# Kernel optimization log

Measured on AMD Instinct MI355X. Metric: run time of the kernel, lower is better.

Reference implementation:

```python
import jax, jax.numpy as jnp
import numpy as np

B, S, D, E = 4, 2048, 1024, 8
HD = D // E          # per-expert head dim = 128
ROPE = HD // 2       # rotary dims = 64 (32 complex pairs)


def setup_inputs() -> dict:
    key = jax.random.key(0)
    ks = jax.random.split(key, 5)
    x = jax.random.normal(ks[0], (B, S, D), dtype=jnp.float32)
    Wg = jax.random.normal(ks[1], (D, E), dtype=jnp.float32) * 0.02
    Wqkv = jax.random.normal(ks[2], (E, D, 3 * HD), dtype=jnp.float32) * 0.02
    Wff = jax.random.normal(ks[3], (E, HD, D), dtype=jnp.float32) * 0.02
    b_ff = jnp.zeros((D,), dtype=jnp.float32)
    # precompute_freqs_cis(qk_rope_head_dim=ROPE, seqlen=S), theta=10000
    inv = 1.0 / (10000.0 ** (np.arange(0, ROPE, 2, dtype=np.float32) / ROPE))  # [ROPE//2]
    ang = np.arange(S, dtype=np.float32)[:, None] * inv[None, :]               # [S, ROPE//2]
    cos = jnp.asarray(np.cos(ang), dtype=jnp.float32)
    sin = jnp.asarray(np.sin(ang), dtype=jnp.float32)
    return {"x": x, "Wg": Wg, "Wqkv": Wqkv, "Wff": Wff, "b_ff": b_ff, "cos": cos, "sin": sin}


def _apply_rope(x, cos, sin):
    # x: [B,S,E,HD]; rotate the second half (x_pe), keep first half (x_nope), cat (pe, nope)
    b, s, e, hd = x.shape
    x_nope, x_pe = x[..., : hd // 2], x[..., hd // 2 :]
    xr = x_pe.reshape(b, s, e, hd // 4, 2)
    re, im = xr[..., 0], xr[..., 1]
    c = cos[None, :, None, :]
    sn = sin[None, :, None, :]
    rot = jnp.stack([re * c - im * sn, re * sn + im * c], axis=-1).reshape(b, s, e, hd // 2)
    return jnp.concatenate([rot, x_nope], axis=-1)


def reference(x, Wg, Wqkv, Wff, b_ff, cos, sin):
    b, s, d = x.shape
    e, hd = Wqkv.shape[0], Wqkv.shape[2] // 3
    # RoPE on per-expert chunks
    xh = _apply_rope(x.reshape(b, s, e, hd), cos, sin).reshape(b, s, d)
    # SwitchGate: top-1 routing
    probs = jax.nn.softmax(xh @ Wg, axis=-1)            # [b,s,E]
    expert = jnp.argmax(probs, axis=-1)                 # [b,s]
    gate = jnp.max(probs, axis=-1)                      # [b,s]
    # preprocess: per-expert stable gather of routed tokens (capacity = s, padded+masked)
    is_e = expert[None, :, :] == jnp.arange(e)[:, None, None]        # [E,b,s] bool
    order = jnp.argsort(jnp.where(is_e, 0, 1), axis=-1, stable=True)  # [E,b,s] routed-first
    mask_g = jnp.take_along_axis(is_e, order, axis=-1).astype(xh.dtype)  # [E,b,s]
    x_g = jnp.take_along_axis(xh[None], order[..., None], axis=2)    # [E,b,s,d]
    gate_g = jnp.take_along_axis(gate[None], order, axis=2)          # [E,b,s]
    # expert-grouped column-parallel QKV
    qkv = jnp.einsum("ebsd,edf->ebsf", x_g, Wqkv)                    # [E,b,s,3*hd]
    q, k, v = jnp.split(qkv, 3, axis=-1)                             # [E,b,s,hd]
    # grouped sparse attention within each expert's token set
    dot = jnp.einsum("ebqh,ebkh->ebqk", q, k) / jnp.sqrt(jnp.asarray(hd, xh.dtype))
    dot = dot - 1e6 * (1.0 - mask_g[:, :, None, :])
    attn = jax.nn.softmax(dot, axis=-1)
    ctx = jnp.einsum("ebqk,ebkh->ebqh", attn, v)                     # [E,b,s,hd]
    # row-parallel output projection, gate-weighted
    out = jnp.einsum("ebsh,ehd->ebsd", ctx, Wff) + b_ff
    out = out * (gate_g * mask_g)[..., None]
    # scatter_add combine back to [b,s,d]
    outs = jnp.zeros((b, s, d), dtype=xh.dtype)
    outs = outs.at[jnp.arange(b)[None, :, None], order].add(out)
    return outs
```

## Files before the change

### kernel.cpp

```cpp
#include <hip/hip_runtime.h>
#include <math.h>

#define Bn 4
#define Sn 2048
#define Dn 1024
#define En 8
#define HDn 128
#define NG 32
#define MAXT 160
#define MAXN 1024

typedef __attribute__((ext_vector_type(8))) short bf16x8;
typedef __attribute__((ext_vector_type(4))) float f32x4;
typedef unsigned short u16;

__device__ __forceinline__ unsigned bf16_rn(float x) {
  unsigned u = __float_as_uint(x);
  return (u + 0x7fffu + ((u >> 16) & 1u)) >> 16;
}
__device__ __forceinline__ void bsplit(float x, unsigned& hi, unsigned& lo) {
  hi = bf16_rn(x);
  lo = bf16_rn(x - __uint_as_float(hi << 16));
}
__device__ __forceinline__ void gl16(const void* g, void* l) {
  __builtin_amdgcn_global_load_lds(
      (const __attribute__((address_space(1))) void*)g,
      (__attribute__((address_space(3))) void*)l, 16, 0, 0);
}
#define MFMA16(a, b, c) __builtin_amdgcn_mfma_f32_16x16x32_bf16((a), (b), (c), 0, 0, 0)

__device__ __forceinline__ void prep_body(
    const float* __restrict__ W, u16* __restrict__ hiT, u16* __restrict__ loT,
    int Kdim, int Ndim, int e, int k0, int c0, float (*tile)[65])
{
  int t = threadIdx.x;
  int r = t >> 4, cc = (t & 15) << 2;
  const float* src = W + ((size_t)e * Kdim + k0) * Ndim + c0;
#pragma unroll
  for (int i = 0; i < 4; ++i) {
    float4 v = *(const float4*)(src + (size_t)(r + i * 16) * Ndim + cc);
    tile[r + i * 16][cc + 0] = v.x; tile[r + i * 16][cc + 1] = v.y;
    tile[r + i * 16][cc + 2] = v.z; tile[r + i * 16][cc + 3] = v.w;
  }
  __syncthreads();
#pragma unroll
  for (int i = 0; i < 4; ++i) {
    int oc = (t >> 4) + i * 16;
    int ok = (t & 15) << 2;
    float v0 = tile[ok + 0][oc], v1 = tile[ok + 1][oc];
    float v2 = tile[ok + 2][oc], v3 = tile[ok + 3][oc];
    unsigned h0,l0,h1,l1,h2,l2,h3,l3;
    bsplit(v0,h0,l0); bsplit(v1,h1,l1); bsplit(v2,h2,l2); bsplit(v3,h3,l3);
    size_t o = ((size_t)e * Ndim + c0 + oc) * Kdim + k0 + ok;
    *(ushort4*)(hiT + o) = make_ushort4((u16)h0,(u16)h1,(u16)h2,(u16)h3);
    *(ushort4*)(loT + o) = make_ushort4((u16)l0,(u16)l1,(u16)l2,(u16)l3);
  }
}

__global__ __launch_bounds__(256) void k_prologue(
    const float* __restrict__ x, const float* __restrict__ Wg,
    const float* __restrict__ cosT, const float* __restrict__ sinT,
    const float* __restrict__ Wqkv, const float* __restrict__ Wff,
    u16* __restrict__ xh_hi, u16* __restrict__ xh_lo,
    u16* __restrict__ WqT_hi, u16* __restrict__ WqT_lo,
    u16* __restrict__ WfT_hi, u16* __restrict__ WfT_lo,
    int* __restrict__ expertArr, float* __restrict__ gateArr,
    int* __restrict__ done)
{
  __shared__ float tile[64][65];
  int bid = blockIdx.x;
  if (bid == 0 && threadIdx.x == 0) done[0] = 0;
  if (bid < 2048) {
    int wid = threadIdx.x >> 6, l = threadIdx.x & 63;
    int bs = (bid << 2) + wid;
    int s  = bs & (Sn - 1);
    const float* xrow = x + (size_t)bs * Dn;
    int j0 = l << 4;
    int hb = j0 & ~127;
    int jj = j0 & 127;
    float v[16];
    if (jj < 64) {
      const float* pe = xrow + hb + 64 + jj;
      float a[16];
      *(float4*)(a + 0)  = *(const float4*)(pe + 0);
      *(float4*)(a + 4)  = *(const float4*)(pe + 4);
      *(float4*)(a + 8)  = *(const float4*)(pe + 8);
      *(float4*)(a + 12) = *(const float4*)(pe + 12);
      int p0 = jj >> 1;
#pragma unroll
      for (int i = 0; i < 8; ++i) {
        float c  = cosT[s * 32 + p0 + i];
        float sn = sinT[s * 32 + p0 + i];
        v[2 * i]     = a[2 * i] * c - a[2 * i + 1] * sn;
        v[2 * i + 1] = a[2 * i] * sn + a[2 * i + 1] * c;
      }
    } else {
      const float* np = xrow + hb + (jj - 64);
      *(float4*)(v + 0)  = *(const float4*)(np + 0);
      *(float4*)(v + 4)  = *(const float4*)(np + 4);
      *(float4*)(v + 8)  = *(const float4*)(np + 8);
      *(float4*)(v + 12) = *(const float4*)(np + 12);
    }
    u16 hh[16] __attribute__((aligned(16)));
    u16 ll[16] __attribute__((aligned(16)));
#pragma unroll
    for (int i = 0; i < 16; ++i) {
      unsigned h, lo;
      bsplit(v[i], h, lo);
      hh[i] = (u16)h; ll[i] = (u16)lo;
    }
    *(uint4*)(xh_hi + (size_t)bs * Dn + j0)     = *(uint4*)(hh);
    *(uint4*)(xh_hi + (size_t)bs * Dn + j0 + 8) = *(uint4*)(hh + 8);
    *(uint4*)(xh_lo + (size_t)bs * Dn + j0)     = *(uint4*)(ll);
    *(uint4*)(xh_lo + (size_t)bs * Dn + j0 + 8) = *(uint4*)(ll + 8);

    float pl[8] = {0.f, 0.f, 0.f, 0.f, 0.f, 0.f, 0.f, 0.f};
    const float* wr = Wg + (size_t)j0 * En;
#pragma unroll
    for (int i = 0; i < 16; ++i) {
      float4 w0 = *(const float4*)(wr + i * 8);
      float4 w1 = *(const float4*)(wr + i * 8 + 4);
      float xv = v[i];
      pl[0] += xv * w0.x; pl[1] += xv * w0.y; pl[2] += xv * w0.z; pl[3] += xv * w0.w;
      pl[4] += xv * w1.x; pl[5] += xv * w1.y; pl[6] += xv * w1.z; pl[7] += xv * w1.w;
    }
#pragma unroll
    for (int off = 1; off < 64; off <<= 1) {
#pragma unroll
      for (int e = 0; e < 8; ++e) pl[e] += __shfl_xor(pl[e], off, 64);
    }
    float m = pl[0]; int be = 0;
#pragma unroll
    for (int e = 1; e < 8; ++e) if (pl[e] > m) { m = pl[e]; be = e; }
    float ss = 0.f;
#pragma unroll
    for (int e = 0; e < 8; ++e) ss += expf(pl[e] - m);
    if (l == 0) {
      expertArr[bs] = be;
      gateArr[bs] = 1.0f / ss;
    }
  } else if (bid < 2048 + 768) {
    int id = bid - 2048;
    int e = id / 96, r2 = id % 96;
    prep_body(Wqkv, WqT_hi, WqT_lo, Dn, 384, e, (r2 / 6) << 6, (r2 % 6) << 6, tile);
  } else {
    int id = bid - 2816;
    int e = id >> 5, r2 = id & 31;
    prep_body(Wff, WfT_hi, WfT_lo, HDn, Dn, e, (r2 >> 4) << 6, (r2 & 15) << 6, tile);
  }
}

__global__ __launch_bounds__(256) void k_route(
    const int* __restrict__ expertArr, int* __restrict__ idx, int* __restrict__ cnt,
    int* __restrict__ tileg, int* __restrict__ tilem, int* __restrict__ ntile,
    int* __restrict__ done)
{
  int g = blockIdx.x;
  int b = g >> 3, e = g & 7;
  int t = threadIdx.x;
  __shared__ int wtot[4];
  __shared__ int base;
  if (t == 0) base = 0;
  __syncthreads();
  for (int c = 0; c < Sn; c += 256) {
    int s = c + t;
    int pred = (expertArr[b * Sn + s] == e) ? 1 : 0;
    unsigned long long mask = __ballot(pred);
    int ln = t & 63, wv = t >> 6;
    int wpre = __popcll(mask & ((1ull << ln) - 1ull));
    if (ln == 63) wtot[wv] = wpre + pred;
    __syncthreads();
    int woff = 0;
    for (int w = 0; w < wv; ++w) woff += wtot[w];
    int tot = wtot[0] + wtot[1] + wtot[2] + wtot[3];
    if (pred) idx[(g << 11) + base + woff + wpre] = s;
    __syncthreads();
    if (t == 0) base += tot;
    __syncthreads();
  }
  if (t == 0) {
    cnt[g] = base;
    __threadfence();
    if (atomicAdd(done, 1) == NG - 1) {
      int tc = 0;
      for (int gg = 0; gg < NG; ++gg) {
        int nn = __hip_atomic_load(&cnt[gg], __ATOMIC_ACQUIRE, __HIP_MEMORY_SCOPE_AGENT);
        for (int m0 = 0; m0 < nn && tc < MAXT; m0 += 64) { tileg[tc] = gg; tilem[tc] = m0; ++tc; }
      }
      ntile[0] = tc;
    }
  }
}

__global__ __launch_bounds__(256) void k_qkv(
    const u16* __restrict__ xh_hi, const u16* __restrict__ xh_lo,
    const u16* __restrict__ WqT_hi, const u16* __restrict__ WqT_lo,
    const int* __restrict__ idx, const int* __restrict__ cnt,
    u16* __restrict__ qkv_hi, u16* __restrict__ qkv_lo,
    u16* __restrict__ vT_hi, u16* __restrict__ vT_lo)
{
  extern __shared__ unsigned char LDS[];
  int bid = blockIdx.x;
  int r8 = bid & 7, q = bid >> 3;
  int g = r8 + ((q & 3) << 3);
  int slot = q >> 2;
  int m0 = (slot >> 1) << 6;
  int n0 = (slot & 1) * 192;
  int n = cnt[g];
  if (m0 >= n) return;
  int b = g >> 3, e = g & 7;
  const int* idxg = idx + (g << 11);
  int t = threadIdx.x;
  int w = t >> 6, l = t & 63;
  int lc = l & 15, lq = l >> 4;

  int srow = t >> 2;
  int sslot = (t & 3) ^ ((srow >> 1) & 3);
  int rgs = m0 + srow; rgs = rgs < n ? rgs : n - 1;
  size_t aoffR = ((size_t)(b * Sn + idxg[rgs])) * Dn + sslot * 8;
  size_t boffR0 = ((size_t)e * 384 + n0 + srow) * Dn + sslot * 8;
  unsigned dst = (unsigned)t << 4;

  f32x4 acc[4][3];
#pragma unroll
  for (int i = 0; i < 4; ++i)
#pragma unroll
    for (int j = 0; j < 3; ++j) acc[i][j] = (f32x4){0.f, 0.f, 0.f, 0.f};

  unsigned off = (unsigned)((lq ^ ((lc >> 1) & 3)) << 4);

#define STAGE(bb, k0)                                                 \
  do {                                                                \
    gl16(xh_hi + aoffR + (k0), LDS + (bb) + dst);                     \
    gl16(xh_lo + aoffR + (k0), LDS + (bb) + 4096 + dst);              \
    gl16(WqT_hi + boffR0 + (k0), LDS + (bb) + 8192 + dst);            \
    gl16(WqT_hi + boffR0 + (size_t)64 * Dn + (k0), LDS + (bb) + 12288 + dst); \
    gl16(WqT_hi + boffR0 + (size_t)128 * Dn + (k0), LDS + (bb) + 16384 + dst);\
    gl16(WqT_lo + boffR0 + (k0), LDS + (bb) + 20480 + dst);           \
    gl16(WqT_lo + boffR0 + (size_t)64 * Dn + (k0), LDS + (bb) + 24576 + dst); \
    gl16(WqT_lo + boffR0 + (size_t)128 * Dn + (k0), LDS + (bb) + 28672 + dst);\
  } while (0)

  STAGE(0, 0);
  asm volatile("s_waitcnt vmcnt(0)" ::: "memory");
  __builtin_amdgcn_s_barrier();
  for (int tt = 0; tt < 32; ++tt) {
    unsigned cur = (tt & 1) ? 32768u : 0u;
    if (tt < 31) {
      STAGE(cur ^ 32768u, (tt + 1) * 32);
      asm volatile("s_waitcnt vmcnt(8)" ::: "memory");
    } else {
      asm volatile("s_waitcnt vmcnt(0)" ::: "memory");
    }
    __builtin_amdgcn_s_barrier();
    bf16x8 ah[4], al[4], bh[3], bl[3];
#pragma unroll
    for (int fi = 0; fi < 4; ++fi) {
      unsigned ab = cur + (unsigned)((fi * 16 + lc) * 64) + off;
      ah[fi] = *(const bf16x8*)(LDS + ab);
      al[fi] = *(const bf16x8*)(LDS + ab + 4096);
    }
#pragma unroll
    for (int fj = 0; fj < 3; ++fj) {
      unsigned bb2 = cur + 8192u + (unsigned)((w * 48 + fj * 16 + lc) * 64) + off;
      bh[fj] = *(const bf16x8*)(LDS + bb2);
      bl[fj] = *(const bf16x8*)(LDS + bb2 + 12288);
    }
#pragma unroll
    for (int fi = 0; fi < 4; ++fi)
#pragma unroll
      for (int fj = 0; fj < 3; ++fj) {
        acc[fi][fj] = MFMA16(ah[fi], bh[fj], acc[fi][fj]);
        acc[fi][fj] = MFMA16(al[fi], bh[fj], acc[fi][fj]);
        acc[fi][fj] = MFMA16(ah[fi], bl[fj], acc[fi][fj]);
      }
    asm volatile("s_waitcnt lgkmcnt(0)" ::: "memory");
    __builtin_amdgcn_sched_barrier(0);
    __builtin_amdgcn_s_barrier();
  }
#undef STAGE

#pragma unroll
  for (int fi = 0; fi < 4; ++fi) {
#pragma unroll
    for (int rr = 0; rr < 4; ++rr) {
      int rg = m0 + fi * 16 + lq * 4 + rr;
      if (rg < n) {
        int tok = idxg[rg];
#pragma unroll
        for (int fj = 0; fj < 3; ++fj) {
          int col = n0 + w * 48 + fj * 16 + lc;
          unsigned h, lo2;
          bsplit(acc[fi][fj][rr], h, lo2);
          if (col < 256) {
            size_t o = (size_t)(b * Sn + tok) * 384 + col;
            qkv_hi[o] = (u16)h; qkv_lo[o] = (u16)lo2;
          } else {
            size_t o = ((size_t)g * HDn + (col - 256)) * MAXN + rg;
            vT_hi[o] = (u16)h; vT_lo[o] = (u16)lo2;
          }
        }
      }
    }
  }
}

__global__ __launch_bounds__(256) void k_attn(
    const u16* __restrict__ qkv_hi, const u16* __restrict__ qkv_lo,
    const u16* __restrict__ vT_hi, const u16* __restrict__ vT_lo,
    const int* __restrict__ idx, const int* __restrict__ cnt,
    const int* __restrict__ tileg, const int* __restrict__ tilem,
    const int* __restrict__ ntile,
    u16* __restrict__ ctx_hi, u16* __restrict__ ctx_lo)
{
  extern __shared__ unsigned char LDS[];
  int tid = blockIdx.x;
  if (tid >= ntile[0]) return;
  int g = tileg[tid], m0 = tilem[tid];
  int n = cnt[g];
  int b = g >> 3;
  const int* idxg = idx + (g << 11);
  int t = threadIdx.x, wid = t >> 6, l = t & 63;
  int lc = l & 15, lq = l >> 4;
  const float scale = 0.08838834764831845f;

  int qrg = m0 + wid * 16 + lc; qrg = qrg < n ? qrg : n - 1;
  size_t qoff = (size_t)(b * Sn + idxg[qrg]) * 384 + lq * 8;
  bf16x8 Qhi[4], Qlo[4];
#pragma unroll
  for (int ks = 0; ks < 4; ++ks) {
    Qhi[ks] = *(const bf16x8*)(qkv_hi + qoff + ks * 32);
    Qlo[ks] = *(const bf16x8*)(qkv_lo + qoff + ks * 32);
  }

  f32x4 acc[8];
#pragma unroll
  for (int i = 0; i < 8; ++i) acc[i] = (f32x4){0.f, 0.f, 0.f, 0.f};
  float m_r[4] = {-1e30f, -1e30f, -1e30f, -1e30f};
  float l_r[4] = {0.f, 0.f, 0.f, 0.f};

  size_t vbase = ((size_t)g * HDn + lc) * MAXN + lq * 8;
  unsigned pbase = 65536u + wid * 4096u;

#define STAGEK(bufb, kc)                                                     \
  do {                                                                       \
    unsigned bb = (bufb);                                                    \
    for (int j = 0; j < 4; ++j) {                                            \
      int c = wid * 4 + j;                                                   \
      int row = (kc) + c * 4 + lq;                                           \
      int rg = row < n ? row : n - 1;                                        \
      int srcslot = lc ^ (((c & 1) << 2) | lq);                              \
      size_t soff = (size_t)(b * Sn + idxg[rg]) * 384 + 128 + srcslot * 8;   \
      gl16(qkv_hi + soff, LDS + bb + c * 1024);                              \
      gl16(qkv_lo + soff, LDS + bb + 16384 + c * 1024);                      \
    }                                                                        \
  } while (0)

  int nt = (n + 63) >> 6;
  STAGEK(0, 0);
  __syncthreads();

  for (int tt = 0; tt < nt; ++tt) {
    unsigned cur = (tt & 1) ? 32768u : 0u;
    if (tt + 1 < nt) STAGEK(cur ^ 32768u, (tt + 1) * 64);
    int kc = tt * 64;

    f32x4 Sf[4];
#pragma unroll
    for (int kf = 0; kf < 4; ++kf) Sf[kf] = (f32x4){0.f, 0.f, 0.f, 0.f};
#pragma unroll
    for (int ks = 0; ks < 4; ++ks) {
#pragma unroll
      for (int kf = 0; kf < 4; ++kf) {
        int row = kf * 16 + lc;
        unsigned byte = cur + row * 256 + ((((ks << 2) | lq) ^ (row & 7)) << 4);
        bf16x8 kh = *(const bf16x8*)(LDS + byte);
        bf16x8 kl = *(const bf16x8*)(LDS + byte + 16384);
        Sf[kf] = MFMA16(Qhi[ks], kh, Sf[kf]);
        Sf[kf] = MFMA16(Qlo[ks], kh, Sf[kf]);
        Sf[kf] = MFMA16(Qhi[ks], kl, Sf[kf]);
      }
    }

    float mloc[4] = {-1e30f, -1e30f, -1e30f, -1e30f};
#pragma unroll
    for (int kf = 0; kf < 4; ++kf) {
#pragma unroll
      for (int r = 0; r < 4; ++r) {
        int key = kc + kf * 16 + lc;
        float s = (key < n) ? Sf[kf][r] * scale : -1e30f;
        Sf[kf][r] = s;
        mloc[r] = fmaxf(mloc[r], s);
      }
    }
#pragma unroll
    for (int off = 1; off < 16; off <<= 1) {
#pragma unroll
      for (int r = 0; r < 4; ++r) mloc[r] = fmaxf(mloc[r], __shfl_xor(mloc[r], off, 64));
    }
    float corr[4], rs[4] = {0.f, 0.f, 0.f, 0.f};
#pragma unroll
    for (int r = 0; r < 4; ++r) {
      float mn = fmaxf(m_r[r], mloc[r]);
      corr[r] = expf(m_r[r] - mn);
      m_r[r] = mn;
    }
#pragma unroll
    for (int kf = 0; kf < 4; ++kf) {
#pragma unroll
      for (int r = 0; r < 4; ++r) {
        float p = expf(Sf[kf][r] - m_r[r]);
        rs[r] += p;
        unsigned ph, plo;
        bsplit(p, ph, plo);
        int prow = (lq << 2) | r;
        int slot = (kf << 1) | (lc >> 3);
        unsigned pb = pbase + prow * 128 + ((slot ^ (prow & 7)) << 4) + ((lc & 7) << 1);
        *(u16*)(LDS + pb) = (u16)ph;
        *(u16*)(LDS + pb + 2048) = (u16)plo;
      }
    }
#pragma unroll
    for (int off = 1; off < 16; off <<= 1) {
#pragma unroll
      for (int r = 0; r < 4; ++r) rs[r] += __shfl_xor(rs[r], off, 64);
    }
#pragma unroll
    for (int r = 0; r < 4; ++r) l_r[r] = l_r[r] * corr[r] + rs[r];
#pragma unroll
    for (int df = 0; df < 8; ++df)
#pragma unroll
      for (int r = 0; r < 4; ++r) acc[df][r] *= corr[r];

#pragma unroll
    for (int ks2 = 0; ks2 < 2; ++ks2) {
      unsigned pr = pbase + lc * 128 + ((((ks2 << 2) | lq) ^ (lc & 7)) << 4);
      bf16x8 pa = *(const bf16x8*)(LDS + pr);
      bf16x8 pl = *(const bf16x8*)(LDS + pr + 2048);
#pragma unroll
      for (int df = 0; df < 8; ++df) {
        size_t vo = vbase + (size_t)(df * 16) * MAXN + kc + ks2 * 32;
        bf16x8 vh = *(const bf16x8*)(vT_hi + vo);
        bf16x8 vl = *(const bf16x8*)(vT_lo + vo);
        acc[df] = MFMA16(pa, vh, acc[df]);
        acc[df] = MFMA16(pl, vh, acc[df]);
        acc[df] = MFMA16(pa, vl, acc[df]);
      }
    }
    __syncthreads();
  }
#undef STAGEK

#pragma unroll
  for (int r = 0; r < 4; ++r) {
    int rg = m0 + wid * 16 + (lq << 2) + r;
    if (rg < n) {
      int tok = idxg[rg];
      float inv = 1.0f / l_r[r];
      size_t o = (size_t)(b * Sn + tok) * HDn + lc;
#pragma unroll
      for (int df = 0; df < 8; ++df) {
        unsigned h, lo2;
        bsplit(acc[df][r] * inv, h, lo2);
        ctx_hi[o + df * 16] = (u16)h;
        ctx_lo[o + df * 16] = (u16)lo2;
      }
    }
  }
}

__global__ __launch_bounds__(256) void k_out(
    const u16* __restrict__ ctx_hi, const u16* __restrict__ ctx_lo,
    const u16* __restrict__ WfT_hi, const u16* __restrict__ WfT_lo,
    const float* __restrict__ bff,
    const int* __restrict__ idx, const int* __restrict__ cnt,
    const int* __restrict__ tileg, const int* __restrict__ tilem,
    const int* __restrict__ ntile,
    const float* __restrict__ gateArr,
    float* __restrict__ out)
{
  int tid = blockIdx.x;
  if (tid >= ntile[0]) return;
  int g = tileg[tid], m0 = tilem[tid];
  int n = cnt[g];
  int b = g >> 3, e = g & 7;
  const int* idxg = idx + (g << 11);
  int t = threadIdx.x, wid = t >> 6, l = t & 63;
  int lc = l & 15, lq = l >> 4;
  int n0 = blockIdx.y * 256 + wid * 64;

  f32x4 acc[4][4];
#pragma unroll
  for (int i = 0; i < 4; ++i)
#pragma unroll
    for (int j = 0; j < 4; ++j) acc[i][j] = (f32x4){0.f, 0.f, 0.f, 0.f};

  size_t aoff[4];
#pragma unroll
  for (int fi = 0; fi < 4; ++fi) {
    int rg = m0 + fi * 16 + lc; rg = rg < n ? rg : n - 1;
    aoff[fi] = ((size_t)(b * Sn + idxg[rg])) * HDn + lq * 8;
  }
  size_t boff[4];
#pragma unroll
  for (int fj = 0; fj < 4; ++fj)
    boff[fj] = ((size_t)e * Dn + n0 + fj * 16 + lc) * HDn + lq * 8;

#pragma unroll
  for (int ks = 0; ks < 4; ++ks) {
    int ko = ks * 32;
    bf16x8 ah[4], al[4], bh[4], bl[4];
#pragma unroll
    for (int fi = 0; fi < 4; ++fi) {
      ah[fi] = *(const bf16x8*)(ctx_hi + aoff[fi] + ko);
      al[fi] = *(const bf16x8*)(ctx_lo + aoff[fi] + ko);
    }
#pragma unroll
    for (int fj = 0; fj < 4; ++fj) {
      bh[fj] = *(const bf16x8*)(WfT_hi + boff[fj] + ko);
      bl[fj] = *(const bf16x8*)(WfT_lo + boff[fj] + ko);
    }
#pragma unroll
    for (int fi = 0; fi < 4; ++fi)
#pragma unroll
      for (int fj = 0; fj < 4; ++fj) {
        acc[fi][fj] = MFMA16(ah[fi], bh[fj], acc[fi][fj]);
        acc[fi][fj] = MFMA16(al[fi], bh[fj], acc[fi][fj]);
        acc[fi][fj] = MFMA16(ah[fi], bl[fj], acc[fi][fj]);
      }
  }

  float bv[4];
#pragma unroll
  for (int fj = 0; fj < 4; ++fj) bv[fj] = bff[n0 + fj * 16 + lc];

#pragma unroll
  for (int fi = 0; fi < 4; ++fi) {
#pragma unroll
    for (int rr = 0; rr < 4; ++rr) {
      int rg = m0 + fi * 16 + lq * 4 + rr;
      if (rg < n) {
        int tok = idxg[rg];
        float gt = gateArr[b * Sn + tok];
        float* orow = out + ((size_t)(b * Sn + tok)) * Dn + n0 + lc;
#pragma unroll
        for (int fj = 0; fj < 4; ++fj)
          orow[fj * 16] = (acc[fi][fj][rr] + bv[fj]) * gt;
      }
    }
  }
}

extern "C" void kernel_launch(void* const* d_in, const int* in_sizes, int n_in,
                              void* d_out, int out_size, void* d_ws, size_t ws_size,
                              hipStream_t stream) {
  const float* x    = (const float*)d_in[0];
  const float* Wg   = (const float*)d_in[1];
  const float* Wqkv = (const float*)d_in[2];
  const float* Wff  = (const float*)d_in[3];
  const float* bff  = (const float*)d_in[4];
  const float* cosT = (const float*)d_in[5];
  const float* sinT = (const float*)d_in[6];
  float* out = (float*)d_out;

  size_t off = 0;
  auto carve = [&](size_t bytes) -> void* {
    void* p = (char*)d_ws + off;
    off += (bytes + 255) & ~(size_t)255;
    return p;
  };
  u16* xh_hi  = (u16*)carve((size_t)Bn * Sn * Dn * 2);
  u16* xh_lo  = (u16*)carve((size_t)Bn * Sn * Dn * 2);
  u16* WqT_hi = (u16*)carve((size_t)En * 384 * Dn * 2);
  u16* WqT_lo = (u16*)carve((size_t)En * 384 * Dn * 2);
  u16* WfT_hi = (u16*)carve((size_t)En * Dn * HDn * 2);
  u16* WfT_lo = (u16*)carve((size_t)En * Dn * HDn * 2);
  u16* qkv_hi = (u16*)carve((size_t)Bn * Sn * 384 * 2);
  u16* qkv_lo = (u16*)carve((size_t)Bn * Sn * 384 * 2);
  u16* vT_hi  = (u16*)carve((size_t)NG * HDn * MAXN * 2);
  u16* vT_lo  = (u16*)carve((size_t)NG * HDn * MAXN * 2);
  u16* ctx_hi = (u16*)carve((size_t)Bn * Sn * HDn * 2);
  u16* ctx_lo = (u16*)carve((size_t)Bn * Sn * HDn * 2);
  float* gateArr = (float*)carve((size_t)Bn * Sn * sizeof(float));
  int*   expertA = (int*)carve((size_t)Bn * Sn * sizeof(int));
  int*   idx     = (int*)carve((size_t)NG * Sn * sizeof(int));
  int*   cnt     = (int*)carve((size_t)NG * sizeof(int));
  int*   tileg   = (int*)carve((size_t)MAXT * sizeof(int));
  int*   tilem   = (int*)carve((size_t)MAXT * sizeof(int));
  int*   ntile   = (int*)carve(256);
  int*   done    = (int*)carve(256);
  (void)ws_size; (void)in_sizes; (void)n_in; (void)out_size;

  hipFuncSetAttribute((const void*)k_attn, hipFuncAttributeMaxDynamicSharedMemorySize, 81920);

  k_prologue<<<dim3(3072), dim3(256), 0, stream>>>(x, Wg, cosT, sinT, Wqkv, Wff,
      xh_hi, xh_lo, WqT_hi, WqT_lo, WfT_hi, WfT_lo, expertA, gateArr, done);
  k_route<<<dim3(NG), dim3(256), 0, stream>>>(expertA, idx, cnt, tileg, tilem, ntile, done);
  k_qkv<<<dim3(384), dim3(256), 65536, stream>>>(xh_hi, xh_lo, WqT_hi, WqT_lo, idx, cnt, qkv_hi, qkv_lo, vT_hi, vT_lo);
  k_attn<<<dim3(MAXT), dim3(256), 81920, stream>>>(qkv_hi, qkv_lo, vT_hi, vT_lo, idx, cnt, tileg, tilem, ntile, ctx_hi, ctx_lo);
  k_out<<<dim3(MAXT, 4), dim3(256), 0, stream>>>(ctx_hi, ctx_lo, WfT_hi, WfT_lo, bff, idx, cnt, tileg, tilem, ntile, gateArr, out);
}
```

Baseline: 186.9 us.

## Vectorize prologue loads, add launch bounds and MFMA priority hints

The prologue kernel gets a min-blocks-per-CU launch bound, vectorized float4 loads of the cos/sin tables in place of scalar loads, and batched loads of the gate weights ahead of the FMAs. In the QKV GEMM and attention kernels, s_setprio raises wave priority around the MFMA blocks so that waves in their matrix phase are scheduled ahead of waves doing loads. The prologue changes target load latency and occupancy, and the priority hints target overlap between waves. Batching eight float4 weight loads raises register pressure, which may conflict with the new occupancy bound.

After: 189.4 us. About the same (+1.3%).

```diff
diff --git a/kernel.cpp b/kernel.cpp
--- a/kernel.cpp
+++ b/kernel.cpp
@@ -57,7 +57,7 @@
   }
 }
 
-__global__ __launch_bounds__(256) void k_prologue(
+__global__ __launch_bounds__(256, 4) void k_prologue(
     const float* __restrict__ x, const float* __restrict__ Wg,
     const float* __restrict__ cosT, const float* __restrict__ sinT,
     const float* __restrict__ Wqkv, const float* __restrict__ Wff,
@@ -87,10 +87,15 @@
       *(float4*)(a + 8)  = *(const float4*)(pe + 8);
       *(float4*)(a + 12) = *(const float4*)(pe + 12);
       int p0 = jj >> 1;
+      float cbuf[8], sbuf[8];
+      *(float4*)(cbuf + 0) = *(const float4*)(cosT + s * 32 + p0);
+      *(float4*)(cbuf + 4) = *(const float4*)(cosT + s * 32 + p0 + 4);
+      *(float4*)(sbuf + 0) = *(const float4*)(sinT + s * 32 + p0);
+      *(float4*)(sbuf + 4) = *(const float4*)(sinT + s * 32 + p0 + 4);
 #pragma unroll
       for (int i = 0; i < 8; ++i) {
-        float c  = cosT[s * 32 + p0 + i];
-        float sn = sinT[s * 32 + p0 + i];
+        float c  = cbuf[i];
+        float sn = sbuf[i];
         v[2 * i]     = a[2 * i] * c - a[2 * i + 1] * sn;
         v[2 * i + 1] = a[2 * i] * sn + a[2 * i + 1] * c;
       }
@@ -117,12 +122,17 @@
     float pl[8] = {0.f, 0.f, 0.f, 0.f, 0.f, 0.f, 0.f, 0.f};
     const float* wr = Wg + (size_t)j0 * En;
 #pragma unroll
-    for (int i = 0; i < 16; ++i) {
-      float4 w0 = *(const float4*)(wr + i * 8);
-      float4 w1 = *(const float4*)(wr + i * 8 + 4);
-      float xv = v[i];
-      pl[0] += xv * w0.x; pl[1] += xv * w0.y; pl[2] += xv * w0.z; pl[3] += xv * w0.w;
-      pl[4] += xv * w1.x; pl[5] += xv * w1.y; pl[6] += xv * w1.z; pl[7] += xv * w1.w;
+    for (int c4 = 0; c4 < 4; ++c4) {
+      float4 wbuf[8];
+#pragma unroll
+      for (int k = 0; k < 8; ++k) wbuf[k] = *(const float4*)(wr + c4 * 32 + k * 4);
+#pragma unroll
+      for (int i2 = 0; i2 < 4; ++i2) {
+        float xv = v[c4 * 4 + i2];
+        float4 w0 = wbuf[i2 * 2], w1 = wbuf[i2 * 2 + 1];
+        pl[0] += xv * w0.x; pl[1] += xv * w0.y; pl[2] += xv * w0.z; pl[3] += xv * w0.w;
+        pl[4] += xv * w1.x; pl[5] += xv * w1.y; pl[6] += xv * w1.z; pl[7] += xv * w1.w;
+      }
     }
 #pragma unroll
     for (int off = 1; off < 64; off <<= 1) {
@@ -266,6 +276,7 @@
       bh[fj] = *(const bf16x8*)(LDS + bb2);
       bl[fj] = *(const bf16x8*)(LDS + bb2 + 12288);
     }
+    __builtin_amdgcn_s_setprio(1);
 #pragma unroll
     for (int fi = 0; fi < 4; ++fi)
 #pragma unroll
@@ -274,6 +285,7 @@
         acc[fi][fj] = MFMA16(al[fi], bh[fj], acc[fi][fj]);
         acc[fi][fj] = MFMA16(ah[fi], bl[fj], acc[fi][fj]);
       }
+    __builtin_amdgcn_s_setprio(0);
     asm volatile("s_waitcnt lgkmcnt(0)" ::: "memory");
     __builtin_amdgcn_sched_barrier(0);
     __builtin_amdgcn_s_barrier();
@@ -368,6 +380,7 @@
     f32x4 Sf[4];
 #pragma unroll
     for (int kf = 0; kf < 4; ++kf) Sf[kf] = (f32x4){0.f, 0.f, 0.f, 0.f};
+    __builtin_amdgcn_s_setprio(1);
 #pragma unroll
     for (int ks = 0; ks < 4; ++ks) {
 #pragma unroll
@@ -381,6 +394,7 @@
         Sf[kf] = MFMA16(Qhi[ks], kl, Sf[kf]);
       }
     }
+    __builtin_amdgcn_s_setprio(0);
 
     float mloc[4] = {-1e30f, -1e30f, -1e30f, -1e30f};
 #pragma unroll
@@ -437,6 +451,7 @@
       unsigned pr = pbase + lc * 128 + ((((ks2 << 2) | lq) ^ (lc & 7)) << 4);
       bf16x8 pa = *(const bf16x8*)(LDS + pr);
       bf16x8 pl = *(const bf16x8*)(LDS + pr + 2048);
+      __builtin_amdgcn_s_setprio(1);
 #pragma unroll
       for (int df = 0; df < 8; ++df) {
         size_t vo = vbase + (size_t)(df * 16) * MAXN + kc + ks2 * 32;
@@ -446,6 +461,7 @@
         acc[df] = MFMA16(pl, vh, acc[df]);
         acc[df] = MFMA16(pa, vl, acc[df]);
       }
+      __builtin_amdgcn_s_setprio(0);
     }
     __syncthreads();
   }
```
